# Optimization experiments

Hardware: AMD Instinct MI355X
Metric: run time of the kernel (lower is better)

## Reference

```python
import jax, jax.numpy as jnp
import numpy as np

B, DIM, SIZE = 16, 512, 128

def _conv2d(x, w, pad_h, pad_w):
    # x: [B,C,H,W], w: [O,I,kh,kw]
    return jax.lax.conv_general_dilated(
        x, w, window_strides=(1, 1),
        padding=((pad_h, pad_h), (pad_w, pad_w)),
        dimension_numbers=('NCHW', 'OIHW', 'NCHW'))


def setup_inputs() -> dict:
    key = jax.random.key(0)
    ks = jax.random.split(key, 8)
    s = SIZE
    return {
        'x': jax.random.normal(ks[0], (B, DIM, s, s), dtype=jnp.float32),
        'w_conv': jax.random.normal(ks[1], (2, DIM, 1, 1), dtype=jnp.float32) * (1.0 / np.sqrt(DIM)),
        'w_ww_conv': jax.random.normal(ks[2], (1, 2, s, 5), dtype=jnp.float32) * (1.0 / np.sqrt(2 * s * 5)),
        'w_hw_conv': jax.random.normal(ks[3], (1, 2, 5, s), dtype=jnp.float32) * (1.0 / np.sqrt(2 * s * 5)),
        'ww_lin_w': jax.random.normal(ks[4], (s, s), dtype=jnp.float32) * (1.0 / np.sqrt(s)),
        'ww_lin_b': jax.random.normal(ks[5], (s,), dtype=jnp.float32) * 0.01,
        'hw_lin_w': jax.random.normal(ks[6], (s, s), dtype=jnp.float32) * (1.0 / np.sqrt(s)),
        'hw_lin_b': jax.random.normal(ks[7], (s,), dtype=jnp.float32) * 0.01,
    }


def reference(x, w_conv, w_ww_conv, w_hw_conv, ww_lin_w, ww_lin_b, hw_lin_w, hw_lin_b):
    # 1x1 conv dim -> 2 (no bias, no bn, no act): pure channel GEMM
    x2 = jnp.einsum('bchw,oc->bohw', x, w_conv[:, :, 0, 0])  # [B,2,S,S]

    # ww branch: conv kernel (SIZE,5), pad (0,2) -> [B,1,1,S]
    ww = _conv2d(x2, w_ww_conv, 0, 2)[:, 0, 0, :]            # [B,S]
    ww = jax.nn.sigmoid(ww @ ww_lin_w.T + ww_lin_b)          # Linear + Sigmoid

    # hw branch: conv kernel (5,SIZE), pad (2,0) -> [B,1,S,1]
    hw = _conv2d(x2, w_hw_conv, 2, 0)[:, 0, :, 0]            # [B,S]
    hw = jax.nn.sigmoid(hw @ hw_lin_w.T + hw_lin_b)

    # batched outer product hw (S,1) @ ww (1,S) -> [B,S,S]
    return jnp.einsum('bh,bw->bhw', hw, ww)
```

## Files before the change

### kernel.cpp

```cpp
#include <hip/hip_runtime.h>
#include <math.h>

#define BB   16
#define CC   512
#define SS   128
#define HWSZ (SS * SS)

__global__ __launch_bounds__(128) void k1_channel_reduce(
    const float* __restrict__ x, const float* __restrict__ wconv,
    float* __restrict__ x2, float* __restrict__ x2t)
{
    __shared__ float wsA[CC];
    __shared__ float wsB[CC];

    const int tid = threadIdx.x;
    for (int i = tid; i < CC; i += 128) {
        wsA[i] = wconv[i];
        wsB[i] = wconv[CC + i];
    }
    __syncthreads();

    const int b  = blockIdx.x >> 5;
    const int tg = blockIdx.x & 31;
    const float* xp = x + (size_t)b * CC * HWSZ + (size_t)tg * (4 * SS) + tid * 4;

    float4 a0 = make_float4(0.f, 0.f, 0.f, 0.f);
    float4 a1 = make_float4(0.f, 0.f, 0.f, 0.f);
    #pragma unroll 8
    for (int c = 0; c < CC; ++c) {
        const float4 v = *(const float4*)(xp + (size_t)c * HWSZ);
        const float wa = wsA[c];
        const float wb = wsB[c];
        a0.x = fmaf(v.x, wa, a0.x); a0.y = fmaf(v.y, wa, a0.y);
        a0.z = fmaf(v.z, wa, a0.z); a0.w = fmaf(v.w, wa, a0.w);
        a1.x = fmaf(v.x, wb, a1.x); a1.y = fmaf(v.y, wb, a1.y);
        a1.z = fmaf(v.z, wb, a1.z); a1.w = fmaf(v.w, wb, a1.w);
    }

    const int hloc = tid >> 5;
    const int w0   = (tid & 31) * 4;
    const int h    = tg * 4 + hloc;

    *(float4*)&x2[((size_t)(b * 2 + 0) * SS + h) * SS + w0] = a0;
    *(float4*)&x2[((size_t)(b * 2 + 1) * SS + h) * SS + w0] = a1;

    x2t[((size_t)(b * 2 + 0) * SS + (w0 + 0)) * SS + h] = a0.x;
    x2t[((size_t)(b * 2 + 0) * SS + (w0 + 1)) * SS + h] = a0.y;
    x2t[((size_t)(b * 2 + 0) * SS + (w0 + 2)) * SS + h] = a0.z;
    x2t[((size_t)(b * 2 + 0) * SS + (w0 + 3)) * SS + h] = a0.w;
    x2t[((size_t)(b * 2 + 1) * SS + (w0 + 0)) * SS + h] = a1.x;
    x2t[((size_t)(b * 2 + 1) * SS + (w0 + 1)) * SS + h] = a1.y;
    x2t[((size_t)(b * 2 + 1) * SS + (w0 + 2)) * SS + h] = a1.z;
    x2t[((size_t)(b * 2 + 1) * SS + (w0 + 3)) * SS + h] = a1.w;
}

__global__ __launch_bounds__(256) void k2_rest(
    const float* __restrict__ x2, const float* __restrict__ x2t,
    const float* __restrict__ wwc,
    const float* __restrict__ hwc,
    const float* __restrict__ wlw, const float* __restrict__ wlb,
    const float* __restrict__ hlw, const float* __restrict__ hlb,
    float* __restrict__ out)
{
    __shared__ float tw[2][5][SS];
    __shared__ float uh[2][5][SS];
    __shared__ float vbuf[2 * SS];
    __shared__ float rbuf[2 * SS];

    const int b        = blockIdx.x;
    const int tid      = threadIdx.x;
    const int lane_pos = tid & 127;
    const int half     = tid >> 7;
    const int half_u   = __builtin_amdgcn_readfirstlane(half);

    {
        const float* xrow = x2 + (size_t)(b * 2 + half) * HWSZ + lane_pos;
        const float* wrow = wwc + half_u * (SS * 5);
        float acc[5] = {0.f, 0.f, 0.f, 0.f, 0.f};
        #pragma unroll 8
        for (int kh = 0; kh < SS; ++kh) {
            const float xv = xrow[(size_t)kh * SS];
            #pragma unroll
            for (int kw = 0; kw < 5; ++kw)
                acc[kw] = fmaf(xv, wrow[kh * 5 + kw], acc[kw]);
        }
        #pragma unroll
        for (int kw = 0; kw < 5; ++kw) tw[half][kw][lane_pos] = acc[kw];
    }

    {
        const float* xcol = x2t + (size_t)(b * 2 + half) * HWSZ + lane_pos;
        const float* wrow = hwc + half_u * (5 * SS);
        float acc[5] = {0.f, 0.f, 0.f, 0.f, 0.f};
        #pragma unroll 8
        for (int kw = 0; kw < SS; ++kw) {
            const float xv = xcol[(size_t)kw * SS];
            #pragma unroll
            for (int kh = 0; kh < 5; ++kh)
                acc[kh] = fmaf(xv, wrow[kh * SS + kw], acc[kh]);
        }
        #pragma unroll
        for (int kh = 0; kh < 5; ++kh) uh[half][kh][lane_pos] = acc[kh];
    }
    __syncthreads();

    {
        float s = 0.f;
        if (half == 0) {
            const int wo = lane_pos;
            #pragma unroll
            for (int kw = 0; kw < 5; ++kw) {
                const int wsrc = wo + kw - 2;
                if (wsrc >= 0 && wsrc < SS) s += tw[0][kw][wsrc] + tw[1][kw][wsrc];
            }
        } else {
            const int ho = lane_pos;
            #pragma unroll
            for (int kh = 0; kh < 5; ++kh) {
                const int hsrc = ho + kh - 2;
                if (hsrc >= 0 && hsrc < SS) s += uh[0][kh][hsrc] + uh[1][kh][hsrc];
            }
        }
        vbuf[tid] = s;
    }
    __syncthreads();

    {
        const int j = lane_pos;
        const float* lw  = (half == 0) ? wlw : hlw;
        const float* lb  = (half == 0) ? wlb : hlb;
        const float* vin = vbuf + half * SS;
        float s = lb[j];
        const float4* wr = (const float4*)(lw + (size_t)j * SS);
        #pragma unroll 4
        for (int k4 = 0; k4 < SS / 4; ++k4) {
            const float4 wv = wr[k4];
            s = fmaf(vin[4 * k4 + 0], wv.x, s);
            s = fmaf(vin[4 * k4 + 1], wv.y, s);
            s = fmaf(vin[4 * k4 + 2], wv.z, s);
            s = fmaf(vin[4 * k4 + 3], wv.w, s);
        }
        rbuf[tid] = 1.f / (1.f + expf(-s));
    }
    __syncthreads();

    {
        float* ob = out + (size_t)b * HWSZ;
        for (int p4 = tid; p4 < HWSZ / 4; p4 += 256) {
            const int h  = p4 >> 5;
            const int w0 = (p4 & 31) * 4;
            const float hv = rbuf[SS + h];
            float4 o;
            o.x = hv * rbuf[w0 + 0];
            o.y = hv * rbuf[w0 + 1];
            o.z = hv * rbuf[w0 + 2];
            o.w = hv * rbuf[w0 + 3];
            *(float4*)(ob + (size_t)h * SS + w0) = o;
        }
    }
}

extern "C" void kernel_launch(void* const* d_in, const int* in_sizes, int n_in,
                              void* d_out, int out_size, void* d_ws, size_t ws_size,
                              hipStream_t stream) {
    const float* x     = (const float*)d_in[0];
    const float* wconv = (const float*)d_in[1];
    const float* wwc   = (const float*)d_in[2];
    const float* hwc   = (const float*)d_in[3];
    const float* wlw   = (const float*)d_in[4];
    const float* wlb   = (const float*)d_in[5];
    const float* hlw   = (const float*)d_in[6];
    const float* hlb   = (const float*)d_in[7];
    float* out = (float*)d_out;

    float* x2  = (float*)d_ws;
    float* x2t = x2 + (size_t)BB * 2 * HWSZ;

    k1_channel_reduce<<<dim3(BB * 32), dim3(128), 0, stream>>>(x, wconv, x2, x2t);
    k2_rest<<<dim3(BB), dim3(256), 0, stream>>>(x2, x2t, wwc, hwc,
                                                wlw, wlb, hlw, hlb, out);
}
```

Measured before the change: 692.9 us.

## Split channel reduction across blocks with partial sums and parallelize conv branches

The single-pass channel reduction over all 512 channels is replaced by a split-K scheme. Each of 256 large blocks reduces a 32-channel slice into a partial buffer, with four independent float4 loads per channel per thread. A second kernel sums the 16 partials and writes both the normal and transposed x2. The tail kernel now runs the ww and hw conv branches on separate thread groups with 512 threads. This targets the low memory-level parallelism of the original streaming kernel, at the cost of an extra launch, roughly 32MB of partial-buffer traffic, and a larger workspace requirement.

```diff
diff --git a/kernel.cpp b/kernel.cpp
--- a/kernel.cpp
+++ b/kernel.cpp
@@ -5,56 +5,85 @@
 #define CC   512
 #define SS   128
 #define HWSZ (SS * SS)
-
-__global__ __launch_bounds__(128) void k1_channel_reduce(
+#define NCH  16
+#define CK   (CC / NCH)
+
+__global__ __launch_bounds__(1024) void k1a_partial(
     const float* __restrict__ x, const float* __restrict__ wconv,
-    float* __restrict__ x2, float* __restrict__ x2t)
+    float* __restrict__ part)
 {
-    __shared__ float wsA[CC];
-    __shared__ float wsB[CC];
-
+    const int b   = blockIdx.x >> 4;
+    const int ck  = blockIdx.x & (NCH - 1);
     const int tid = threadIdx.x;
-    for (int i = tid; i < CC; i += 128) {
-        wsA[i] = wconv[i];
-        wsB[i] = wconv[CC + i];
-    }
-    __syncthreads();
-
-    const int b  = blockIdx.x >> 5;
-    const int tg = blockIdx.x & 31;
-    const float* xp = x + (size_t)b * CC * HWSZ + (size_t)tg * (4 * SS) + tid * 4;
-
-    float4 a0 = make_float4(0.f, 0.f, 0.f, 0.f);
-    float4 a1 = make_float4(0.f, 0.f, 0.f, 0.f);
-    #pragma unroll 8
-    for (int c = 0; c < CC; ++c) {
-        const float4 v = *(const float4*)(xp + (size_t)c * HWSZ);
-        const float wa = wsA[c];
-        const float wb = wsB[c];
-        a0.x = fmaf(v.x, wa, a0.x); a0.y = fmaf(v.y, wa, a0.y);
-        a0.z = fmaf(v.z, wa, a0.z); a0.w = fmaf(v.w, wa, a0.w);
-        a1.x = fmaf(v.x, wb, a1.x); a1.y = fmaf(v.y, wb, a1.y);
-        a1.z = fmaf(v.z, wb, a1.z); a1.w = fmaf(v.w, wb, a1.w);
-    }
-
-    const int hloc = tid >> 5;
-    const int w0   = (tid & 31) * 4;
-    const int h    = tg * 4 + hloc;
-
-    *(float4*)&x2[((size_t)(b * 2 + 0) * SS + h) * SS + w0] = a0;
-    *(float4*)&x2[((size_t)(b * 2 + 1) * SS + h) * SS + w0] = a1;
-
-    x2t[((size_t)(b * 2 + 0) * SS + (w0 + 0)) * SS + h] = a0.x;
-    x2t[((size_t)(b * 2 + 0) * SS + (w0 + 1)) * SS + h] = a0.y;
-    x2t[((size_t)(b * 2 + 0) * SS + (w0 + 2)) * SS + h] = a0.z;
-    x2t[((size_t)(b * 2 + 0) * SS + (w0 + 3)) * SS + h] = a0.w;
-    x2t[((size_t)(b * 2 + 1) * SS + (w0 + 0)) * SS + h] = a1.x;
-    x2t[((size_t)(b * 2 + 1) * SS + (w0 + 1)) * SS + h] = a1.y;
-    x2t[((size_t)(b * 2 + 1) * SS + (w0 + 2)) * SS + h] = a1.z;
-    x2t[((size_t)(b * 2 + 1) * SS + (w0 + 3)) * SS + h] = a1.w;
-}
-
-__global__ __launch_bounds__(256) void k2_rest(
+
+    const float* xp = x + ((size_t)b * CC + (size_t)ck * CK) * HWSZ + tid * 4;
+    const float* wA = wconv + ck * CK;
+    const float* wB = wconv + CC + ck * CK;
+
+    float4 a0[4], a1[4];
+    #pragma unroll
+    for (int s = 0; s < 4; ++s) {
+        a0[s] = make_float4(0.f, 0.f, 0.f, 0.f);
+        a1[s] = make_float4(0.f, 0.f, 0.f, 0.f);
+    }
+
+    #pragma unroll 2
+    for (int c = 0; c < CK; ++c) {
+        const float wa = wA[c];
+        const float wb = wB[c];
+        #pragma unroll
+        for (int s = 0; s < 4; ++s) {
+            const float4 v = *(const float4*)(xp + (size_t)c * HWSZ + s * 4096);
+            a0[s].x = fmaf(v.x, wa, a0[s].x);
+            a0[s].y = fmaf(v.y, wa, a0[s].y);
+            a0[s].z = fmaf(v.z, wa, a0[s].z);
+            a0[s].w = fmaf(v.w, wa, a0[s].w);
+            a1[s].x = fmaf(v.x, wb, a1[s].x);
+            a1[s].y = fmaf(v.y, wb, a1[s].y);
+            a1[s].z = fmaf(v.z, wb, a1[s].z);
+            a1[s].w = fmaf(v.w, wb, a1[s].w);
+        }
+    }
+
+    float* pp = part + (size_t)(b * NCH + ck) * 2 * HWSZ + tid * 4;
+    #pragma unroll
+    for (int s = 0; s < 4; ++s) {
+        *(float4*)(pp + s * 4096)        = a0[s];
+        *(float4*)(pp + HWSZ + s * 4096) = a1[s];
+    }
+}
+
+__global__ __launch_bounds__(256) void k1b_reduce(
+    const float* __restrict__ part, float* __restrict__ x2,
+    float* __restrict__ x2t)
+{
+    const int pc  = blockIdx.x & 15;
+    const int o   = (blockIdx.x >> 4) & 1;
+    const int b   = blockIdx.x >> 5;
+    const int tid = threadIdx.x;
+
+    const int p = (pc * 256 + tid) * 4;
+
+    const float* pp = part + ((size_t)(b * NCH) * 2 + o) * HWSZ + p;
+    float4 s = make_float4(0.f, 0.f, 0.f, 0.f);
+    #pragma unroll
+    for (int ck = 0; ck < NCH; ++ck) {
+        const float4 v = *(const float4*)(pp + (size_t)ck * 2 * HWSZ);
+        s.x += v.x; s.y += v.y; s.z += v.z; s.w += v.w;
+    }
+
+    *(float4*)&x2[(size_t)(b * 2 + o) * HWSZ + p] = s;
+
+    const int h  = p >> 7;
+    const int w0 = p & 127;
+    float* t = x2t + ((size_t)(b * 2 + o) * SS + w0) * SS + h;
+    t[0 * SS] = s.x;
+    t[1 * SS] = s.y;
+    t[2 * SS] = s.z;
+    t[3 * SS] = s.w;
+}
+
+__global__ __launch_bounds__(512) void k2_rest(
     const float* __restrict__ x2, const float* __restrict__ x2t,
     const float* __restrict__ wwc,
     const float* __restrict__ hwc,
@@ -70,10 +99,11 @@
     const int b        = blockIdx.x;
     const int tid      = threadIdx.x;
     const int lane_pos = tid & 127;
-    const int half     = tid >> 7;
+    const int q        = tid >> 7;
+    const int half     = q & 1;
     const int half_u   = __builtin_amdgcn_readfirstlane(half);
 
-    {
+    if (q < 2) {
         const float* xrow = x2 + (size_t)(b * 2 + half) * HWSZ + lane_pos;
         const float* wrow = wwc + half_u * (SS * 5);
         float acc[5] = {0.f, 0.f, 0.f, 0.f, 0.f};
@@ -86,9 +116,7 @@
         }
         #pragma unroll
         for (int kw = 0; kw < 5; ++kw) tw[half][kw][lane_pos] = acc[kw];
-    }
-
-    {
+    } else {
         const float* xcol = x2t + (size_t)(b * 2 + half) * HWSZ + lane_pos;
         const float* wrow = hwc + half_u * (5 * SS);
         float acc[5] = {0.f, 0.f, 0.f, 0.f, 0.f};
@@ -104,7 +132,7 @@
     }
     __syncthreads();
 
-    {
+    if (tid < 256) {
         float s = 0.f;
         if (half == 0) {
             const int wo = lane_pos;
@@ -125,7 +153,7 @@
     }
     __syncthreads();
 
-    {
+    if (tid < 256) {
         const int j = lane_pos;
         const float* lw  = (half == 0) ? wlw : hlw;
         const float* lb  = (half == 0) ? wlb : hlb;
@@ -146,7 +174,7 @@
 
     {
         float* ob = out + (size_t)b * HWSZ;
-        for (int p4 = tid; p4 < HWSZ / 4; p4 += 256) {
+        for (int p4 = tid; p4 < HWSZ / 4; p4 += 512) {
             const int h  = p4 >> 5;
             const int w0 = (p4 & 31) * 4;
             const float hv = rbuf[SS + h];
@@ -173,10 +201,12 @@
     const float* hlb   = (const float*)d_in[7];
     float* out = (float*)d_out;
 
-    float* x2  = (float*)d_ws;
-    float* x2t = x2 + (size_t)BB * 2 * HWSZ;
-
-    k1_channel_reduce<<<dim3(BB * 32), dim3(128), 0, stream>>>(x, wconv, x2, x2t);
-    k2_rest<<<dim3(BB), dim3(256), 0, stream>>>(x2, x2t, wwc, hwc,
+    float* x2   = (float*)d_ws;
+    float* x2t  = x2 + (size_t)BB * 2 * HWSZ;
+    float* part = x2t + (size_t)BB * 2 * HWSZ;
+
+    k1a_partial<<<dim3(BB * NCH), dim3(1024), 0, stream>>>(x, wconv, part);
+    k1b_reduce<<<dim3(BB * 2 * 16), dim3(256), 0, stream>>>(part, x2, x2t);
+    k2_rest<<<dim3(BB), dim3(512), 0, stream>>>(x2, x2t, wwc, hwc,
                                                 wlw, wlb, hlw, hlb, out);
 }
```

After: 707.9 us. 2.2% more time.
